# Kernel optimization log

Measured on AMD Instinct MI355X. Metric: run time of the kernel, lower is better.

## Reference

```python
import jax, jax.numpy as jnp
import numpy as np

HIDDEN = 1024
HEADS = 16
HEAD_DIM = HIDDEN // HEADS  # 64
BLOCK = 1024  # block_size; seq_len > BLOCK triggers ring path
B, S = 1, 4096


def setup_inputs() -> dict:
    key = jax.random.key(0)
    k0, k1, k2, k3, k4 = jax.random.split(key, 5)
    w_scale = 0.02
    return {
        "hidden_states": jax.random.normal(k0, (B, S, HIDDEN), dtype=jnp.float32),
        # weights stored [in, out]; applied as x @ W (equivalent to nn.Linear with W.T)
        "w_q": jax.random.normal(k1, (HIDDEN, HIDDEN), dtype=jnp.float32) * w_scale,
        "w_k": jax.random.normal(k2, (HIDDEN, HIDDEN), dtype=jnp.float32) * w_scale,
        "w_v": jax.random.normal(k3, (HIDDEN, HIDDEN), dtype=jnp.float32) * w_scale,
        "w_o": jax.random.normal(k4, (HIDDEN, HIDDEN), dtype=jnp.float32) * w_scale,
    }


def _ring_attention(q, k, v, block, scale):
    # q,k,v: [B, H, S, D]. Faithful to the torch module: each KV block subtracts
    # its OWN local max (no running-max rescale); exp-sums and weighted-V are
    # accumulated additively across KV blocks, then normalized once at the end.
    b, h, s, d = q.shape
    nb = s // block
    kb = jnp.moveaxis(k.reshape(b, h, nb, block, d), 2, 0)  # [nb, B, H, block, D]
    vb = jnp.moveaxis(v.reshape(b, h, nb, block, d), 2, 0)

    def step(carry, kv):
        num, den = carry
        k_blk, v_blk = kv
        s_blk = jnp.einsum("bhqd,bhkd->bhqk", q, k_blk) * scale  # [B,H,S,block]
        m = jnp.max(s_blk, axis=-1, keepdims=True)               # local max only
        e = jnp.exp(s_blk - m)
        num = num + jnp.einsum("bhqk,bhkd->bhqd", e, v_blk)
        den = den + jnp.sum(e, axis=-1, keepdims=True)
        return (num, den), None

    init = (jnp.zeros_like(q), jnp.zeros((b, h, s, 1), dtype=q.dtype))
    (num, den), _ = jax.lax.scan(step, init, (kb, vb))
    return num / den


def reference(hidden_states, w_q, w_k, w_v, w_o):
    b, s, _ = hidden_states.shape
    q = (hidden_states @ w_q).reshape(b, s, HEADS, HEAD_DIM).transpose(0, 2, 1, 3)
    k = (hidden_states @ w_k).reshape(b, s, HEADS, HEAD_DIM).transpose(0, 2, 1, 3)
    v = (hidden_states @ w_v).reshape(b, s, HEADS, HEAD_DIM).transpose(0, 2, 1, 3)
    scale = HEAD_DIM ** -0.5
    out = _ring_attention(q, k, v, BLOCK, scale)          # [B,H,S,D]
    out = out.transpose(0, 2, 1, 3).reshape(b, s, HIDDEN)  # [B,S,hidden]
    return out @ w_o
```

## Files before the change

kernel.cpp:

```cpp
#include <hip/hip_runtime.h>
#include <hip/hip_bf16.h>

typedef __bf16 bf16;
typedef bf16 bf16x2 __attribute__((ext_vector_type(2)));
typedef bf16 bf16x4 __attribute__((ext_vector_type(4)));
typedef bf16 bf16x8 __attribute__((ext_vector_type(8)));
typedef float f32x4 __attribute__((ext_vector_type(4)));

#define HID 1024
#define NHEADS 16
#define HD 64
#define SEQ 4096

__device__ __forceinline__ void gll16(const void* g, void* l) {
  __builtin_amdgcn_global_load_lds(
      (const __attribute__((address_space(1))) void*)g,
      (__attribute__((address_space(3))) void*)l, 16, 0, 0);
}

__global__ __launch_bounds__(256)
void prep_kernel(const float* __restrict__ X,
                 const float* __restrict__ Wq, const float* __restrict__ Wk,
                 const float* __restrict__ Wv, const float* __restrict__ Wo,
                 bf16* __restrict__ Xb, bf16* __restrict__ Wt)
{
  const int z = blockIdx.z, t = threadIdx.x, bx = blockIdx.x;
  if (z == 0) {
    const float4* src = (const float4*)X;
    const int gid = bx * 256 + t;
    #pragma unroll
    for (int i = 0; i < 16; ++i) {
      float4 v = src[gid + i * 65536];
      bf16x4 o = {(bf16)v.x, (bf16)v.y, (bf16)v.z, (bf16)v.w};
      *(bf16x4*)&Xb[(size_t)(gid + i * 65536) * 4] = o;
    }
  } else {
    const float* W = (z == 1) ? Wq : (z == 2) ? Wk : (z == 3) ? Wv : Wo;
    bf16* dst = Wt + (size_t)(z - 1) * HID * HID;
    const float scale = (z == 1) ? 0.125f : 1.0f;
    __shared__ bf16 T[64][68];
    const int tr = (bx >> 4) * 64, tc = (bx & 15) * 64;
    #pragma unroll
    for (int p = 0; p < 4; ++p) {
      int row = (t >> 4) + p * 16;
      float4 v = *(const float4*)&W[(size_t)(tr + row) * HID + tc + (t & 15) * 4];
      T[row][(t & 15) * 4 + 0] = (bf16)(v.x * scale);
      T[row][(t & 15) * 4 + 1] = (bf16)(v.y * scale);
      T[row][(t & 15) * 4 + 2] = (bf16)(v.z * scale);
      T[row][(t & 15) * 4 + 3] = (bf16)(v.w * scale);
    }
    __syncthreads();
    #pragma unroll
    for (int p = 0; p < 4; ++p) {
      int rp = (t >> 4) + p * 16;
      int cb = (t & 15) * 4;
      bf16x4 o = {T[cb + 0][rp], T[cb + 1][rp], T[cb + 2][rp], T[cb + 3][rp]};
      *(bf16x4*)&dst[(size_t)(tc + rp) * HID + tr + cb] = o;
    }
  }
}

__global__ __launch_bounds__(256)
void qkv_gemm(const bf16* __restrict__ A, const bf16* __restrict__ Wt,
              bf16* __restrict__ Qg, bf16* __restrict__ Kg,
              bf16* __restrict__ Vt)
{
  __shared__ bf16 sbuf[16384];
  bf16* As = sbuf;
  bf16* Bs = sbuf + 8192;

  const int t = threadIdx.x, lane = t & 63, w = t >> 6;
  const int z = blockIdx.z;
  const int n0 = blockIdx.x * 128, m0 = blockIdx.y * 128;
  const bf16* Bt = Wt + (size_t)z * HID * HID;
  const int wm = (w & 1) * 64, wn = (w >> 1) * 64;
  const int fr = lane & 15, quad = lane >> 4;

  f32x4 acc[4][4] = {};

  const int sr = lane >> 3;
  const int sc = ((lane & 7) - sr) & 7;
  const bf16* ga = A  + (size_t)(m0 + w * 32 + sr) * HID + sc * 8;
  const bf16* gb = Bt + (size_t)(n0 + w * 32 + sr) * HID + sc * 8;

  for (int k0 = 0; k0 < HID; k0 += 64) {
    __syncthreads();
    #pragma unroll
    for (int c = 0; c < 4; ++c) {
      gll16(ga + (size_t)(c * 8) * HID + k0, As + (w * 32 + c * 8) * 64);
      gll16(gb + (size_t)(c * 8) * HID + k0, Bs + (w * 32 + c * 8) * 64);
    }
    __syncthreads();
    #pragma unroll
    for (int ks = 0; ks < 2; ++ks) {
      bf16x8 af[4], bg[4];
      #pragma unroll
      for (int i = 0; i < 4; ++i)
        af[i] = *(const bf16x8*)&As[(wm + i * 16 + fr) * 64 +
                                    ((ks * 4 + quad + fr) & 7) * 8];
      #pragma unroll
      for (int i = 0; i < 4; ++i)
        bg[i] = *(const bf16x8*)&Bs[(wn + i * 16 + fr) * 64 +
                                    ((ks * 4 + quad + fr) & 7) * 8];
      #pragma unroll
      for (int mi = 0; mi < 4; ++mi)
        #pragma unroll
        for (int ni = 0; ni < 4; ++ni)
          acc[mi][ni] = __builtin_amdgcn_mfma_f32_16x16x32_bf16(
              af[mi], bg[ni], acc[mi][ni], 0, 0, 0);
    }
  }

  if (z < 2) {
    bf16* C = z ? Kg : Qg;
    #pragma unroll
    for (int mi = 0; mi < 4; ++mi)
      #pragma unroll
      for (int ni = 0; ni < 4; ++ni)
        #pragma unroll
        for (int r = 0; r < 4; ++r)
          C[(size_t)(m0 + wm + mi * 16 + quad * 4 + r) * HID +
            n0 + wn + ni * 16 + fr] = (bf16)acc[mi][ni][r];
  } else {
    __syncthreads();
    #pragma unroll
    for (int mi = 0; mi < 4; ++mi)
      #pragma unroll
      for (int ni = 0; ni < 4; ++ni)
        #pragma unroll
        for (int r = 0; r < 4; ++r) {
          int row = wn + ni * 16 + fr;
          int col = wm + mi * 16 + quad * 4 + r;
          int colS = (col + 8 * (row & 15)) & 127;
          sbuf[row * 128 + colS] = (bf16)acc[mi][ni][r];
        }
    __syncthreads();
    const int row = t >> 1, cb = (t & 1) * 64;
    #pragma unroll
    for (int j = 0; j < 8; ++j) {
      int c0 = (cb + j * 8 + 8 * (row & 15)) & 127;
      *(bf16x8*)&Vt[(size_t)(n0 + row) * SEQ + m0 + cb + j * 8] =
          *(const bf16x8*)&sbuf[row * 128 + c0];
    }
  }
}

__global__ __launch_bounds__(256)
void oproj_gemm(const bf16* __restrict__ A, const bf16* __restrict__ Bt,
                float* __restrict__ C)
{
  __shared__ bf16 sbuf[16384];
  bf16* As = sbuf;
  bf16* Bs = sbuf + 8192;

  const int t = threadIdx.x, lane = t & 63, w = t >> 6;
  const int n0 = blockIdx.x * 128, m0 = blockIdx.y * 128;
  const int wm = (w & 1) * 64, wn = (w >> 1) * 64;
  const int fr = lane & 15, quad = lane >> 4;

  f32x4 acc[4][4] = {};

  const int sr = lane >> 3;
  const int sc = ((lane & 7) - sr) & 7;
  const bf16* ga = A  + (size_t)(m0 + w * 32 + sr) * HID + sc * 8;
  const bf16* gb = Bt + (size_t)(n0 + w * 32 + sr) * HID + sc * 8;

  for (int k0 = 0; k0 < HID; k0 += 64) {
    __syncthreads();
    #pragma unroll
    for (int c = 0; c < 4; ++c) {
      gll16(ga + (size_t)(c * 8) * HID + k0, As + (w * 32 + c * 8) * 64);
      gll16(gb + (size_t)(c * 8) * HID + k0, Bs + (w * 32 + c * 8) * 64);
    }
    __syncthreads();
    #pragma unroll
    for (int ks = 0; ks < 2; ++ks) {
      bf16x8 af[4], bg[4];
      #pragma unroll
      for (int i = 0; i < 4; ++i)
        af[i] = *(const bf16x8*)&As[(wm + i * 16 + fr) * 64 +
                                    ((ks * 4 + quad + fr) & 7) * 8];
      #pragma unroll
      for (int i = 0; i < 4; ++i)
        bg[i] = *(const bf16x8*)&Bs[(wn + i * 16 + fr) * 64 +
                                    ((ks * 4 + quad + fr) & 7) * 8];
      #pragma unroll
      for (int mi = 0; mi < 4; ++mi)
        #pragma unroll
        for (int ni = 0; ni < 4; ++ni)
          acc[mi][ni] = __builtin_amdgcn_mfma_f32_16x16x32_bf16(
              af[mi], bg[ni], acc[mi][ni], 0, 0, 0);
    }
  }

  #pragma unroll
  for (int mi = 0; mi < 4; ++mi)
    #pragma unroll
    for (int ni = 0; ni < 4; ++ni)
      #pragma unroll
      for (int r = 0; r < 4; ++r)
        C[(size_t)(m0 + wm + mi * 16 + quad * 4 + r) * HID +
          n0 + wn + ni * 16 + fr] = acc[mi][ni][r];
}

__global__ __launch_bounds__(256)
void attn3(const bf16* __restrict__ Q, const bf16* __restrict__ K,
           const bf16* __restrict__ Vt, bf16* __restrict__ O)
{
  __shared__ bf16 Ks[2][4096];
  __shared__ bf16 Vs[2][4096];
  __shared__ bf16 Ps[4][2048];

  const int t = threadIdx.x, lane = t & 63, w = t >> 6;
  const int h = blockIdx.y, q0 = blockIdx.x * 128;
  const int fr = lane & 15, quad = lane >> 4;

  bf16x8 bq[2][2];
  #pragma unroll
  for (int qf = 0; qf < 2; ++qf)
    #pragma unroll
    for (int ks = 0; ks < 2; ++ks)
      bq[qf][ks] = *(const bf16x8*)&Q[(size_t)(q0 + w * 32 + qf * 16 + fr) * HID
                                      + h * 64 + ks * 32 + quad * 8];

  const int sr = lane >> 3;
  const int sc = ((lane & 7) - sr) & 7;
  const bf16* gk = K  + (size_t)(w * 16 + sr) * HID + h * 64 + sc * 8;
  const bf16* gv = Vt + (size_t)(h * 64 + w * 16 + sr) * SEQ + sc * 8;

  #pragma unroll
  for (int j = 0; j < 2; ++j) {
    gll16(gk + (size_t)(j * 8) * HID, &Ks[0][(w * 16 + j * 8) * 64]);
    gll16(gv + (size_t)(j * 8) * SEQ, &Vs[0][(w * 16 + j * 8) * 64]);
  }

  f32x4 accN[2][4] = {};
  f32x4 accO[2][4] = {};
  float m_i[2] = {-3e38f, -3e38f}, l_i[2] = {0.f, 0.f}, den[2] = {0.f, 0.f};

  __syncthreads();

  for (int kk = 0; kk < 64; ++kk) {
    const int buf = kk & 1;
    if (kk < 63) {
      const size_t key0n = (size_t)(kk + 1) * 64;
      #pragma unroll
      for (int j = 0; j < 2; ++j) {
        gll16(gk + (key0n + j * 8) * HID, &Ks[buf ^ 1][(w * 16 + j * 8) * 64]);
        gll16(gv + key0n + (size_t)(j * 8) * SEQ,
              &Vs[buf ^ 1][(w * 16 + j * 8) * 64]);
      }
    }

    bf16x8 ak[4][2];
    #pragma unroll
    for (int mt = 0; mt < 4; ++mt)
      #pragma unroll
      for (int ks = 0; ks < 2; ++ks)
        ak[mt][ks] = *(const bf16x8*)&Ks[buf][(mt * 16 + fr) * 64 +
                                             ((ks * 4 + quad + fr) & 7) * 8];

    #pragma unroll
    for (int qf = 0; qf < 2; ++qf) {
      f32x4 s[4];
      #pragma unroll
      for (int mt = 0; mt < 4; ++mt) {
        f32x4 z = {};
        z = __builtin_amdgcn_mfma_f32_16x16x32_bf16(ak[mt][0], bq[qf][0], z, 0, 0, 0);
        z = __builtin_amdgcn_mfma_f32_16x16x32_bf16(ak[mt][1], bq[qf][1], z, 0, 0, 0);
        s[mt] = z;
      }
      float mx = -3e38f;
      #pragma unroll
      for (int mt = 0; mt < 4; ++mt)
        #pragma unroll
        for (int r = 0; r < 4; ++r) mx = fmaxf(mx, s[mt][r]);
      mx = fmaxf(mx, __shfl_xor(mx, 16));
      mx = fmaxf(mx, __shfl_xor(mx, 32));
      const float mnew = fmaxf(m_i[qf], mx);
      const float alpha = __expf(m_i[qf] - mnew);
      m_i[qf] = mnew;
      float sum = 0.f;
      const int prow = (qf * 16 + fr) * 64;
      #pragma unroll
      for (int mt = 0; mt < 4; ++mt) {
        float p0 = __expf(s[mt][0] - mnew);
        float p1 = __expf(s[mt][1] - mnew);
        float p2 = __expf(s[mt][2] - mnew);
        float p3 = __expf(s[mt][3] - mnew);
        sum += (p0 + p1) + (p2 + p3);
        bf16x4 pv = {(bf16)p0, (bf16)p1, (bf16)p2, (bf16)p3};
        *(bf16x4*)&Ps[w][prow + ((mt * 2 + (quad >> 1) + fr) & 7) * 8 +
                         (quad & 1) * 4] = pv;
      }
      sum += __shfl_xor(sum, 16);
      sum += __shfl_xor(sum, 32);
      l_i[qf] = l_i[qf] * alpha + sum;
      #pragma unroll
      for (int dt = 0; dt < 4; ++dt) accO[qf][dt] *= alpha;
    }

    #pragma unroll
    for (int ks = 0; ks < 2; ++ks) {
      bf16x8 bp0 = *(const bf16x8*)&Ps[w][fr * 64 +
                                          ((ks * 4 + quad + fr) & 7) * 8];
      bf16x8 bp1 = *(const bf16x8*)&Ps[w][(16 + fr) * 64 +
                                          ((ks * 4 + quad + fr) & 7) * 8];
      #pragma unroll
      for (int dt = 0; dt < 4; ++dt) {
        bf16x8 av = *(const bf16x8*)&Vs[buf][(dt * 16 + fr) * 64 +
                                            ((ks * 4 + quad + fr) & 7) * 8];
        accO[0][dt] = __builtin_amdgcn_mfma_f32_16x16x32_bf16(av, bp0, accO[0][dt], 0, 0, 0);
        accO[1][dt] = __builtin_amdgcn_mfma_f32_16x16x32_bf16(av, bp1, accO[1][dt], 0, 0, 0);
      }
    }

    if ((kk & 15) == 15) {
      #pragma unroll
      for (int qf = 0; qf < 2; ++qf) {
        #pragma unroll
        for (int dt = 0; dt < 4; ++dt) {
          #pragma unroll
          for (int r = 0; r < 4; ++r) accN[qf][dt][r] += accO[qf][dt][r];
          accO[qf][dt] = (f32x4){0.f, 0.f, 0.f, 0.f};
        }
        den[qf] += l_i[qf];
        l_i[qf] = 0.f;
        m_i[qf] = -3e38f;
      }
    }
    __syncthreads();
  }

  #pragma unroll
  for (int qf = 0; qf < 2; ++qf) {
    const float inv = 1.0f / den[qf];
    const size_t orow = (size_t)(q0 + w * 32 + qf * 16 + fr) * HID + h * 64;
    #pragma unroll
    for (int dt = 0; dt < 4; ++dt) {
      bf16x4 ov = {(bf16)(accN[qf][dt][0] * inv), (bf16)(accN[qf][dt][1] * inv),
                   (bf16)(accN[qf][dt][2] * inv), (bf16)(accN[qf][dt][3] * inv)};
      *(bf16x4*)&O[orow + dt * 16 + quad * 4] = ov;
    }
  }
}

extern "C" void kernel_launch(void* const* d_in, const int* in_sizes, int n_in,
                              void* d_out, int out_size, void* d_ws, size_t ws_size,
                              hipStream_t stream)
{
  const float* X  = (const float*)d_in[0];
  const float* Wq = (const float*)d_in[1];
  const float* Wk = (const float*)d_in[2];
  const float* Wv = (const float*)d_in[3];
  const float* Wo = (const float*)d_in[4];
  float* out = (float*)d_out;

  const size_t MB = 1024 * 1024;
  bf16* Xb  = (bf16*)d_ws;
  bf16* Wt  = (bf16*)((char*)d_ws + 8  * MB);
  bf16* Qg  = (bf16*)((char*)d_ws + 16 * MB);
  bf16* Kg  = (bf16*)((char*)d_ws + 24 * MB);
  bf16* Vtg = (bf16*)((char*)d_ws + 32 * MB);
  bf16* Og  = (bf16*)((char*)d_ws + 40 * MB);

  prep_kernel<<<dim3(256, 1, 5), 256, 0, stream>>>(X, Wq, Wk, Wv, Wo, Xb, Wt);
  qkv_gemm<<<dim3(HID / 128, SEQ / 128, 3), 256, 0, stream>>>(Xb, Wt, Qg, Kg, Vtg);
  attn3<<<dim3(SEQ / 128, NHEADS), 256, 0, stream>>>(Qg, Kg, Vtg, Og);
  oproj_gemm<<<dim3(HID / 128, SEQ / 128), 256, 0, stream>>>(
      Og, Wt + (size_t)3 * HID * HID, out);
}
```

Measured before the change: 276.0 us.

## Use 8 waves per attention block, exp2 softmax, and lazy max rescaling

The attention kernel now runs 512 threads per block, with each wave owning 16 query rows instead of 32. This halves per-wave register state and raises the number of waves available to hide latency. The softmax folds log2(e) into the Q weight scale and uses a native exp2. The running-max rescale of the accumulators is skipped unless the block max grows by more than a threshold. A true max is tracked so each 1024-key block is still normalised to its own local max before being added in. The lazy rescale risks larger intermediate exponent values, bounded by the threshold.

```diff
diff --git a/kernel.cpp b/kernel.cpp
--- a/kernel.cpp
+++ b/kernel.cpp
@@ -18,6 +18,14 @@
       (__attribute__((address_space(3))) void*)l, 16, 0, 0);
 }
 
+__device__ __forceinline__ float fast_exp2(float x) {
+#if __has_builtin(__builtin_amdgcn_exp2f)
+  return __builtin_amdgcn_exp2f(x);
+#else
+  return __expf(x * 0.6931471805599453f);
+#endif
+}
+
 __global__ __launch_bounds__(256)
 void prep_kernel(const float* __restrict__ X,
                  const float* __restrict__ Wq, const float* __restrict__ Wk,
@@ -37,7 +45,7 @@
   } else {
     const float* W = (z == 1) ? Wq : (z == 2) ? Wk : (z == 3) ? Wv : Wo;
     bf16* dst = Wt + (size_t)(z - 1) * HID * HID;
-    const float scale = (z == 1) ? 0.125f : 1.0f;
+    const float scale = (z == 1) ? 0.18033688011112042f : 1.0f;
     __shared__ bf16 T[64][68];
     const int tr = (bx >> 4) * 64, tc = (bx & 15) * 64;
     #pragma unroll
@@ -203,40 +211,37 @@
           n0 + wn + ni * 16 + fr] = acc[mi][ni][r];
 }
 
-__global__ __launch_bounds__(256)
-void attn3(const bf16* __restrict__ Q, const bf16* __restrict__ K,
+#define THR_L2 12.0f
+
+__global__ __launch_bounds__(512, 4)
+void attn4(const bf16* __restrict__ Q, const bf16* __restrict__ K,
            const bf16* __restrict__ Vt, bf16* __restrict__ O)
 {
   __shared__ bf16 Ks[2][4096];
   __shared__ bf16 Vs[2][4096];
-  __shared__ bf16 Ps[4][2048];
+  __shared__ bf16 Ps[8][1024];
 
   const int t = threadIdx.x, lane = t & 63, w = t >> 6;
   const int h = blockIdx.y, q0 = blockIdx.x * 128;
   const int fr = lane & 15, quad = lane >> 4;
 
-  bf16x8 bq[2][2];
+  bf16x8 bq[2];
   #pragma unroll
-  for (int qf = 0; qf < 2; ++qf)
-    #pragma unroll
-    for (int ks = 0; ks < 2; ++ks)
-      bq[qf][ks] = *(const bf16x8*)&Q[(size_t)(q0 + w * 32 + qf * 16 + fr) * HID
-                                      + h * 64 + ks * 32 + quad * 8];
+  for (int ks = 0; ks < 2; ++ks)
+    bq[ks] = *(const bf16x8*)&Q[(size_t)(q0 + w * 16 + fr) * HID
+                                + h * 64 + ks * 32 + quad * 8];
 
   const int sr = lane >> 3;
   const int sc = ((lane & 7) - sr) & 7;
-  const bf16* gk = K  + (size_t)(w * 16 + sr) * HID + h * 64 + sc * 8;
-  const bf16* gv = Vt + (size_t)(h * 64 + w * 16 + sr) * SEQ + sc * 8;
-
-  #pragma unroll
-  for (int j = 0; j < 2; ++j) {
-    gll16(gk + (size_t)(j * 8) * HID, &Ks[0][(w * 16 + j * 8) * 64]);
-    gll16(gv + (size_t)(j * 8) * SEQ, &Vs[0][(w * 16 + j * 8) * 64]);
-  }
-
-  f32x4 accN[2][4] = {};
-  f32x4 accO[2][4] = {};
-  float m_i[2] = {-3e38f, -3e38f}, l_i[2] = {0.f, 0.f}, den[2] = {0.f, 0.f};
+  const bf16* gk = K  + (size_t)(w * 8 + sr) * HID + h * 64 + sc * 8;
+  const bf16* gv = Vt + (size_t)(h * 64 + w * 8 + sr) * SEQ + sc * 8;
+
+  gll16(gk, &Ks[0][(w * 8) * 64]);
+  gll16(gv, &Vs[0][(w * 8) * 64]);
+
+  f32x4 accN[4] = {};
+  f32x4 accO[4] = {};
+  float m_used = -3e38f, m_true = -3e38f, l_i = 0.f, den = 0.f;
 
   __syncthreads();
 
@@ -244,12 +249,8 @@
     const int buf = kk & 1;
     if (kk < 63) {
       const size_t key0n = (size_t)(kk + 1) * 64;
-      #pragma unroll
-      for (int j = 0; j < 2; ++j) {
-        gll16(gk + (key0n + j * 8) * HID, &Ks[buf ^ 1][(w * 16 + j * 8) * 64]);
-        gll16(gv + key0n + (size_t)(j * 8) * SEQ,
-              &Vs[buf ^ 1][(w * 16 + j * 8) * 64]);
-      }
+      gll16(gk + key0n * HID, &Ks[buf ^ 1][(w * 8) * 64]);
+      gll16(gv + key0n,       &Vs[buf ^ 1][(w * 8) * 64]);
     }
 
     bf16x8 ak[4][2];
@@ -260,88 +261,83 @@
         ak[mt][ks] = *(const bf16x8*)&Ks[buf][(mt * 16 + fr) * 64 +
                                              ((ks * 4 + quad + fr) & 7) * 8];
 
-    #pragma unroll
-    for (int qf = 0; qf < 2; ++qf) {
-      f32x4 s[4];
-      #pragma unroll
-      for (int mt = 0; mt < 4; ++mt) {
-        f32x4 z = {};
-        z = __builtin_amdgcn_mfma_f32_16x16x32_bf16(ak[mt][0], bq[qf][0], z, 0, 0, 0);
-        z = __builtin_amdgcn_mfma_f32_16x16x32_bf16(ak[mt][1], bq[qf][1], z, 0, 0, 0);
-        s[mt] = z;
-      }
-      float mx = -3e38f;
-      #pragma unroll
-      for (int mt = 0; mt < 4; ++mt)
-        #pragma unroll
-        for (int r = 0; r < 4; ++r) mx = fmaxf(mx, s[mt][r]);
-      mx = fmaxf(mx, __shfl_xor(mx, 16));
-      mx = fmaxf(mx, __shfl_xor(mx, 32));
-      const float mnew = fmaxf(m_i[qf], mx);
-      const float alpha = __expf(m_i[qf] - mnew);
-      m_i[qf] = mnew;
-      float sum = 0.f;
-      const int prow = (qf * 16 + fr) * 64;
-      #pragma unroll
-      for (int mt = 0; mt < 4; ++mt) {
-        float p0 = __expf(s[mt][0] - mnew);
-        float p1 = __expf(s[mt][1] - mnew);
-        float p2 = __expf(s[mt][2] - mnew);
-        float p3 = __expf(s[mt][3] - mnew);
-        sum += (p0 + p1) + (p2 + p3);
-        bf16x4 pv = {(bf16)p0, (bf16)p1, (bf16)p2, (bf16)p3};
-        *(bf16x4*)&Ps[w][prow + ((mt * 2 + (quad >> 1) + fr) & 7) * 8 +
-                         (quad & 1) * 4] = pv;
-      }
-      sum += __shfl_xor(sum, 16);
-      sum += __shfl_xor(sum, 32);
-      l_i[qf] = l_i[qf] * alpha + sum;
-      #pragma unroll
-      for (int dt = 0; dt < 4; ++dt) accO[qf][dt] *= alpha;
-    }
+    f32x4 s[4];
+    #pragma unroll
+    for (int mt = 0; mt < 4; ++mt) {
+      f32x4 z = {};
+      z = __builtin_amdgcn_mfma_f32_16x16x32_bf16(ak[mt][0], bq[0], z, 0, 0, 0);
+      z = __builtin_amdgcn_mfma_f32_16x16x32_bf16(ak[mt][1], bq[1], z, 0, 0, 0);
+      s[mt] = z;
+    }
+
+    float mx0 = fmaxf(fmaxf(s[0][0], s[0][1]), fmaxf(s[0][2], s[0][3]));
+    float mx1 = fmaxf(fmaxf(s[1][0], s[1][1]), fmaxf(s[1][2], s[1][3]));
+    float mx2 = fmaxf(fmaxf(s[2][0], s[2][1]), fmaxf(s[2][2], s[2][3]));
+    float mx3 = fmaxf(fmaxf(s[3][0], s[3][1]), fmaxf(s[3][2], s[3][3]));
+    float mx = fmaxf(fmaxf(mx0, mx1), fmaxf(mx2, mx3));
+    mx = fmaxf(mx, __shfl_xor(mx, 16));
+    mx = fmaxf(mx, __shfl_xor(mx, 32));
+    m_true = fmaxf(m_true, mx);
+
+    if (__any(mx > m_used + THR_L2)) {
+      const float mn = fmaxf(m_used, mx);
+      const float a = fast_exp2(m_used - mn);
+      m_used = mn;
+      l_i *= a;
+      #pragma unroll
+      for (int dt = 0; dt < 4; ++dt) accO[dt] *= a;
+    }
+
+    float sum = 0.f;
+    const int prow = fr * 64;
+    #pragma unroll
+    for (int mt = 0; mt < 4; ++mt) {
+      float p0 = fast_exp2(s[mt][0] - m_used);
+      float p1 = fast_exp2(s[mt][1] - m_used);
+      float p2 = fast_exp2(s[mt][2] - m_used);
+      float p3 = fast_exp2(s[mt][3] - m_used);
+      sum += (p0 + p1) + (p2 + p3);
+      bf16x4 pv = {(bf16)p0, (bf16)p1, (bf16)p2, (bf16)p3};
+      *(bf16x4*)&Ps[w][prow + ((mt * 2 + (quad >> 1) + fr) & 7) * 8 +
+                       (quad & 1) * 4] = pv;
+    }
+    sum += __shfl_xor(sum, 16);
+    sum += __shfl_xor(sum, 32);
+    l_i += sum;
 
     #pragma unroll
     for (int ks = 0; ks < 2; ++ks) {
-      bf16x8 bp0 = *(const bf16x8*)&Ps[w][fr * 64 +
-                                          ((ks * 4 + quad + fr) & 7) * 8];
-      bf16x8 bp1 = *(const bf16x8*)&Ps[w][(16 + fr) * 64 +
-                                          ((ks * 4 + quad + fr) & 7) * 8];
+      bf16x8 bp = *(const bf16x8*)&Ps[w][fr * 64 +
+                                         ((ks * 4 + quad + fr) & 7) * 8];
       #pragma unroll
       for (int dt = 0; dt < 4; ++dt) {
         bf16x8 av = *(const bf16x8*)&Vs[buf][(dt * 16 + fr) * 64 +
                                             ((ks * 4 + quad + fr) & 7) * 8];
-        accO[0][dt] = __builtin_amdgcn_mfma_f32_16x16x32_bf16(av, bp0, accO[0][dt], 0, 0, 0);
-        accO[1][dt] = __builtin_amdgcn_mfma_f32_16x16x32_bf16(av, bp1, accO[1][dt], 0, 0, 0);
+        accO[dt] = __builtin_amdgcn_mfma_f32_16x16x32_bf16(av, bp, accO[dt], 0, 0, 0);
       }
     }
 
     if ((kk & 15) == 15) {
-      #pragma unroll
-      for (int qf = 0; qf < 2; ++qf) {
-        #pragma unroll
-        for (int dt = 0; dt < 4; ++dt) {
-          #pragma unroll
-          for (int r = 0; r < 4; ++r) accN[qf][dt][r] += accO[qf][dt][r];
-          accO[qf][dt] = (f32x4){0.f, 0.f, 0.f, 0.f};
-        }
-        den[qf] += l_i[qf];
-        l_i[qf] = 0.f;
-        m_i[qf] = -3e38f;
-      }
-    }
-    __syncthreads();
-  }
-
+      const float c = fast_exp2(m_used - m_true);
+      den += l_i * c;
+      #pragma unroll
+      for (int dt = 0; dt < 4; ++dt)
+        #pragma unroll
+        for (int r = 0; r < 4; ++r) accN[dt][r] += accO[dt][r] * c;
+      #pragma unroll
+      for (int dt = 0; dt < 4; ++dt) accO[dt] = (f32x4){0.f, 0.f, 0.f, 0.f};
+      l_i = 0.f; m_used = -3e38f; m_true = -3e38f;
+    }
+    __syncthreads();
+  }
+
+  const float inv = 1.0f / den;
+  const size_t orow = (size_t)(q0 + w * 16 + fr) * HID + h * 64;
   #pragma unroll
-  for (int qf = 0; qf < 2; ++qf) {
-    const float inv = 1.0f / den[qf];
-    const size_t orow = (size_t)(q0 + w * 32 + qf * 16 + fr) * HID + h * 64;
-    #pragma unroll
-    for (int dt = 0; dt < 4; ++dt) {
-      bf16x4 ov = {(bf16)(accN[qf][dt][0] * inv), (bf16)(accN[qf][dt][1] * inv),
-                   (bf16)(accN[qf][dt][2] * inv), (bf16)(accN[qf][dt][3] * inv)};
-      *(bf16x4*)&O[orow + dt * 16 + quad * 4] = ov;
-    }
+  for (int dt = 0; dt < 4; ++dt) {
+    bf16x4 ov = {(bf16)(accN[dt][0] * inv), (bf16)(accN[dt][1] * inv),
+                 (bf16)(accN[dt][2] * inv), (bf16)(accN[dt][3] * inv)};
+    *(bf16x4*)&O[orow + dt * 16 + quad * 4] = ov;
   }
 }
 
@@ -366,7 +362,7 @@
 
   prep_kernel<<<dim3(256, 1, 5), 256, 0, stream>>>(X, Wq, Wk, Wv, Wo, Xb, Wt);
   qkv_gemm<<<dim3(HID / 128, SEQ / 128, 3), 256, 0, stream>>>(Xb, Wt, Qg, Kg, Vtg);
-  attn3<<<dim3(SEQ / 128, NHEADS), 256, 0, stream>>>(Qg, Kg, Vtg, Og);
+  attn4<<<dim3(SEQ / 128, NHEADS), 512, 0, stream>>>(Qg, Kg, Vtg, Og);
   oproj_gemm<<<dim3(HID / 128, SEQ / 128), 256, 0, stream>>>(
       Og, Wt + (size_t)3 * HID * HID, out);
 }
```

Result: faster. 250.9 us (-9.1%).

## Use exp2 with folded log2e scale and lazy max rescaling in attention

Applied to the files above, without the earlier changes.

Folds log2(e) into the Q weight scale so softmax exponentials use the native exp2 instruction directly. Online-softmax rescaling of the accumulator is skipped unless the new block max exceeds the current reference by more than a threshold, with a correction to the true max at each KV-block boundary. The P scratch buffer is halved by reusing one 16-row slice per query fragment, and launch bounds ask for two workgroups per CU. This cuts exp and rescale ALU work and LDS use, at the cost of a larger range in the unnormalised exponentials and a tighter register budget.

```diff
diff --git a/kernel.cpp b/kernel.cpp
--- a/kernel.cpp
+++ b/kernel.cpp
@@ -18,6 +18,14 @@
       (__attribute__((address_space(3))) void*)l, 16, 0, 0);
 }
 
+__device__ __forceinline__ float fast_exp2(float x) {
+#if __has_builtin(__builtin_amdgcn_exp2f)
+  return __builtin_amdgcn_exp2f(x);
+#else
+  return __expf(x * 0.6931471805599453f);
+#endif
+}
+
 __global__ __launch_bounds__(256)
 void prep_kernel(const float* __restrict__ X,
                  const float* __restrict__ Wq, const float* __restrict__ Wk,
@@ -37,7 +45,7 @@
   } else {
     const float* W = (z == 1) ? Wq : (z == 2) ? Wk : (z == 3) ? Wv : Wo;
     bf16* dst = Wt + (size_t)(z - 1) * HID * HID;
-    const float scale = (z == 1) ? 0.125f : 1.0f;
+    const float scale = (z == 1) ? 0.18033688011112042f : 1.0f;
     __shared__ bf16 T[64][68];
     const int tr = (bx >> 4) * 64, tc = (bx & 15) * 64;
     #pragma unroll
@@ -203,13 +211,15 @@
           n0 + wn + ni * 16 + fr] = acc[mi][ni][r];
 }
 
-__global__ __launch_bounds__(256)
-void attn3(const bf16* __restrict__ Q, const bf16* __restrict__ K,
+#define THR_L2 12.0f
+
+__global__ __launch_bounds__(256, 2)
+void attn5(const bf16* __restrict__ Q, const bf16* __restrict__ K,
            const bf16* __restrict__ Vt, bf16* __restrict__ O)
 {
   __shared__ bf16 Ks[2][4096];
   __shared__ bf16 Vs[2][4096];
-  __shared__ bf16 Ps[4][2048];
+  __shared__ bf16 Ps[4][1024];
 
   const int t = threadIdx.x, lane = t & 63, w = t >> 6;
   const int h = blockIdx.y, q0 = blockIdx.x * 128;
@@ -236,7 +246,8 @@
 
   f32x4 accN[2][4] = {};
   f32x4 accO[2][4] = {};
-  float m_i[2] = {-3e38f, -3e38f}, l_i[2] = {0.f, 0.f}, den[2] = {0.f, 0.f};
+  float m_used[2] = {-3e38f, -3e38f}, m_true[2] = {-3e38f, -3e38f};
+  float l_i[2] = {0.f, 0.f}, den[2] = {0.f, 0.f};
 
   __syncthreads();
 
@@ -260,34 +271,46 @@
         ak[mt][ks] = *(const bf16x8*)&Ks[buf][(mt * 16 + fr) * 64 +
                                              ((ks * 4 + quad + fr) & 7) * 8];
 
-    #pragma unroll
-    for (int qf = 0; qf < 2; ++qf) {
-      f32x4 s[4];
+    f32x4 s[2][4];
+    #pragma unroll
+    for (int qf = 0; qf < 2; ++qf)
       #pragma unroll
       for (int mt = 0; mt < 4; ++mt) {
         f32x4 z = {};
         z = __builtin_amdgcn_mfma_f32_16x16x32_bf16(ak[mt][0], bq[qf][0], z, 0, 0, 0);
         z = __builtin_amdgcn_mfma_f32_16x16x32_bf16(ak[mt][1], bq[qf][1], z, 0, 0, 0);
-        s[mt] = z;
-      }
-      float mx = -3e38f;
-      #pragma unroll
-      for (int mt = 0; mt < 4; ++mt)
-        #pragma unroll
-        for (int r = 0; r < 4; ++r) mx = fmaxf(mx, s[mt][r]);
+        s[qf][mt] = z;
+      }
+
+    bf16x8 bp[2][2];
+    #pragma unroll
+    for (int qf = 0; qf < 2; ++qf) {
+      float mx0 = fmaxf(fmaxf(s[qf][0][0], s[qf][0][1]), fmaxf(s[qf][0][2], s[qf][0][3]));
+      float mx1 = fmaxf(fmaxf(s[qf][1][0], s[qf][1][1]), fmaxf(s[qf][1][2], s[qf][1][3]));
+      float mx2 = fmaxf(fmaxf(s[qf][2][0], s[qf][2][1]), fmaxf(s[qf][2][2], s[qf][2][3]));
+      float mx3 = fmaxf(fmaxf(s[qf][3][0], s[qf][3][1]), fmaxf(s[qf][3][2], s[qf][3][3]));
+      float mx = fmaxf(fmaxf(mx0, mx1), fmaxf(mx2, mx3));
       mx = fmaxf(mx, __shfl_xor(mx, 16));
       mx = fmaxf(mx, __shfl_xor(mx, 32));
-      const float mnew = fmaxf(m_i[qf], mx);
-      const float alpha = __expf(m_i[qf] - mnew);
-      m_i[qf] = mnew;
+      m_true[qf] = fmaxf(m_true[qf], mx);
+
+      if (__any(mx > m_used[qf] + THR_L2)) {
+        const float mn = fmaxf(m_used[qf], mx);
+        const float a = fast_exp2(m_used[qf] - mn);
+        m_used[qf] = mn;
+        l_i[qf] *= a;
+        #pragma unroll
+        for (int dt = 0; dt < 4; ++dt) accO[qf][dt] *= a;
+      }
+
       float sum = 0.f;
-      const int prow = (qf * 16 + fr) * 64;
+      const int prow = fr * 64;
       #pragma unroll
       for (int mt = 0; mt < 4; ++mt) {
-        float p0 = __expf(s[mt][0] - mnew);
-        float p1 = __expf(s[mt][1] - mnew);
-        float p2 = __expf(s[mt][2] - mnew);
-        float p3 = __expf(s[mt][3] - mnew);
+        float p0 = fast_exp2(s[qf][mt][0] - m_used[qf]);
+        float p1 = fast_exp2(s[qf][mt][1] - m_used[qf]);
+        float p2 = fast_exp2(s[qf][mt][2] - m_used[qf]);
+        float p3 = fast_exp2(s[qf][mt][3] - m_used[qf]);
         sum += (p0 + p1) + (p2 + p3);
         bf16x4 pv = {(bf16)p0, (bf16)p1, (bf16)p2, (bf16)p3};
         *(bf16x4*)&Ps[w][prow + ((mt * 2 + (quad >> 1) + fr) & 7) * 8 +
@@ -295,38 +318,36 @@
       }
       sum += __shfl_xor(sum, 16);
       sum += __shfl_xor(sum, 32);
-      l_i[qf] = l_i[qf] * alpha + sum;
-      #pragma unroll
-      for (int dt = 0; dt < 4; ++dt) accO[qf][dt] *= alpha;
-    }
-
-    #pragma unroll
-    for (int ks = 0; ks < 2; ++ks) {
-      bf16x8 bp0 = *(const bf16x8*)&Ps[w][fr * 64 +
-                                          ((ks * 4 + quad + fr) & 7) * 8];
-      bf16x8 bp1 = *(const bf16x8*)&Ps[w][(16 + fr) * 64 +
-                                          ((ks * 4 + quad + fr) & 7) * 8];
+      l_i[qf] += sum;
+
+      #pragma unroll
+      for (int ks = 0; ks < 2; ++ks)
+        bp[qf][ks] = *(const bf16x8*)&Ps[w][fr * 64 +
+                                            ((ks * 4 + quad + fr) & 7) * 8];
+    }
+
+    #pragma unroll
+    for (int ks = 0; ks < 2; ++ks)
       #pragma unroll
       for (int dt = 0; dt < 4; ++dt) {
         bf16x8 av = *(const bf16x8*)&Vs[buf][(dt * 16 + fr) * 64 +
                                             ((ks * 4 + quad + fr) & 7) * 8];
-        accO[0][dt] = __builtin_amdgcn_mfma_f32_16x16x32_bf16(av, bp0, accO[0][dt], 0, 0, 0);
-        accO[1][dt] = __builtin_amdgcn_mfma_f32_16x16x32_bf16(av, bp1, accO[1][dt], 0, 0, 0);
-      }
-    }
+        accO[0][dt] = __builtin_amdgcn_mfma_f32_16x16x32_bf16(av, bp[0][ks], accO[0][dt], 0, 0, 0);
+        accO[1][dt] = __builtin_amdgcn_mfma_f32_16x16x32_bf16(av, bp[1][ks], accO[1][dt], 0, 0, 0);
+      }
 
     if ((kk & 15) == 15) {
       #pragma unroll
       for (int qf = 0; qf < 2; ++qf) {
-        #pragma unroll
-        for (int dt = 0; dt < 4; ++dt) {
+        const float c = fast_exp2(m_used[qf] - m_true[qf]);
+        den[qf] += l_i[qf] * c;
+        #pragma unroll
+        for (int dt = 0; dt < 4; ++dt)
           #pragma unroll
-          for (int r = 0; r < 4; ++r) accN[qf][dt][r] += accO[qf][dt][r];
-          accO[qf][dt] = (f32x4){0.f, 0.f, 0.f, 0.f};
-        }
-        den[qf] += l_i[qf];
-        l_i[qf] = 0.f;
-        m_i[qf] = -3e38f;
+          for (int r = 0; r < 4; ++r) accN[qf][dt][r] += accO[qf][dt][r] * c;
+        #pragma unroll
+        for (int dt = 0; dt < 4; ++dt) accO[qf][dt] = (f32x4){0.f, 0.f, 0.f, 0.f};
+        l_i[qf] = 0.f; m_used[qf] = -3e38f; m_true[qf] = -3e38f;
       }
     }
     __syncthreads();
@@ -366,7 +387,7 @@
 
   prep_kernel<<<dim3(256, 1, 5), 256, 0, stream>>>(X, Wq, Wk, Wv, Wo, Xb, Wt);
   qkv_gemm<<<dim3(HID / 128, SEQ / 128, 3), 256, 0, stream>>>(Xb, Wt, Qg, Kg, Vtg);
-  attn3<<<dim3(SEQ / 128, NHEADS), 256, 0, stream>>>(Qg, Kg, Vtg, Og);
+  attn5<<<dim3(SEQ / 128, NHEADS), 256, 0, stream>>>(Qg, Kg, Vtg, Og);
   oproj_gemm<<<dim3(HID / 128, SEQ / 128), 256, 0, stream>>>(
       Og, Wt + (size_t)3 * HID * HID, out);
 }
```

Measured after the change: 263.2 us. -4.6%, faster.
